# Performance work log

Measured on AMD Instinct MI355X. Metric: run time of the kernel, lower is better.

The kernel has to match this reference:

```python
import jax, jax.numpy as jnp
import numpy as np
from jax import lax

B, T = 64, 200
NUM_C, DIM_S, SIZE_M = 2000, 128, 50


def setup_inputs() -> dict:
    key = jax.random.key(0)
    ks = jax.random.split(key, 12)
    d = {}
    d['skill'] = jax.random.randint(ks[0], (B, T), 0, NUM_C)
    d['answer'] = jax.random.randint(ks[1], (B, T), 0, 2)
    s = 1.0 / np.sqrt(DIM_S)
    d['k_emb'] = jax.random.normal(ks[2], (NUM_C + 1, DIM_S), jnp.float32)
    d['v_emb'] = jax.random.normal(ks[3], (2 * NUM_C + 1, DIM_S), jnp.float32)
    # kaiming_normal on [size_m, dim_s]: std = sqrt(2/dim_s)
    d['Mk'] = jax.random.normal(ks[4], (SIZE_M, DIM_S), jnp.float32) * np.sqrt(2.0 / DIM_S)
    d['Mv0'] = jax.random.normal(ks[5], (SIZE_M, DIM_S), jnp.float32) * np.sqrt(2.0 / DIM_S)
    d['f_W'] = jax.random.normal(ks[6], (DIM_S, 2 * DIM_S), jnp.float32) * (1.0 / np.sqrt(2 * DIM_S))
    d['f_b'] = jnp.zeros((DIM_S,), jnp.float32)
    d['p_W'] = jax.random.normal(ks[7], (NUM_C, DIM_S), jnp.float32) * s
    d['p_b'] = jnp.zeros((NUM_C,), jnp.float32)
    d['e_W'] = jax.random.normal(ks[8], (DIM_S, DIM_S), jnp.float32) * s
    d['e_b'] = jnp.zeros((DIM_S,), jnp.float32)
    d['a_W'] = jax.random.normal(ks[9], (DIM_S, DIM_S), jnp.float32) * s
    d['a_b'] = jnp.zeros((DIM_S,), jnp.float32)
    return d


def reference(skill, answer, k_emb, v_emb, Mk, Mv0, f_W, f_b, p_W, p_b, e_W, e_b, a_W, a_b):
    num_c = p_W.shape[0]
    bsz = skill.shape[0]
    answer_x = jnp.where(answer == 2, 1, answer)
    x = skill + num_c * answer_x                       # [B,T]
    k = k_emb[skill]                                   # [B,T,D]
    v = v_emb[x]                                       # [B,T,D]
    w = jax.nn.softmax(jnp.einsum('btd,md->btm', k, Mk), axis=-1)   # [B,T,M]
    e = jax.nn.sigmoid(jnp.einsum('btd,ed->bte', v, e_W) + e_b)      # [B,T,D]
    a = jnp.tanh(jnp.einsum('btd,ed->bte', v, a_W) + a_b)            # [B,T,D]

    Mv_init = jnp.broadcast_to(Mv0, (bsz,) + Mv0.shape)              # [B,M,D]

    def step(Mvt, inp):
        et, at, wt = inp                               # [B,D],[B,D],[B,M]
        # read uses pre-update memory (Mv[:, :-1] in the torch code)
        read = jnp.einsum('bm,bmd->bd', wt, Mvt)
        Mvt_new = Mvt * (1.0 - wt[:, :, None] * et[:, None, :]) + wt[:, :, None] * at[:, None, :]
        return Mvt_new, read

    _, reads = lax.scan(step, Mv_init,
                        (e.transpose(1, 0, 2), a.transpose(1, 0, 2), w.transpose(1, 0, 2)))
    reads = reads.transpose(1, 0, 2)                   # [B,T,D]

    f = jnp.tanh(jnp.concatenate([reads, k], axis=-1) @ f_W.T + f_b)  # [B,T,D]
    p = jax.nn.sigmoid(f @ p_W.T + p_b)                # [B,T,num_c] (dropout is identity at eval)
    p = p[:, :-1, :]
    next_skill = skill[:, 1:]                          # [B,T-1]
    idx = jnp.minimum(next_skill, num_c - 1)
    pred = jnp.take_along_axis(p, idx[..., None], axis=-1)[..., 0]
    pred = jnp.where(next_skill < num_c, pred, 0.0)    # index num_c -> zero row in torch one_hot
    return pred
```

## Files before the change

### kernel.cpp

```cpp
#include <hip/hip_runtime.h>
#include <math.h>

#define Bsz 64
#define Tn 200
#define NUMC 2000
#define DS 128
#define SM 50
#define NTOK (Bsz*Tn)

typedef __attribute__((ext_vector_type(8))) short bfrag;
typedef __attribute__((ext_vector_type(4))) float f32x4;
typedef __attribute__((ext_vector_type(4))) unsigned int u32x4;

__device__ __forceinline__ unsigned short f2bf(float x) {
    unsigned int u = __builtin_bit_cast(unsigned int, x);
    u = u + 0x7fffu + ((u >> 16) & 1u);
    return (unsigned short)(u >> 16);
}
__device__ __forceinline__ unsigned int pack2(float a, float b) {
    return (unsigned int)f2bf(a) | ((unsigned int)f2bf(b) << 16);
}
__device__ __forceinline__ bfrag mk_frag(f32x4 x, f32x4 y) {
    u32x4 t;
    t[0] = pack2(x[0], x[1]); t[1] = pack2(x[2], x[3]);
    t[2] = pack2(y[0], y[1]); t[3] = pack2(y[2], y[3]);
    return __builtin_bit_cast(bfrag, t);
}

__device__ __forceinline__ float fast_exp(float x)  { return __builtin_amdgcn_exp2f(x * 1.44269504f); }
__device__ __forceinline__ float fast_rcp(float x)  { return __builtin_amdgcn_rcpf(x); }
__device__ __forceinline__ float fast_sigmoid(float x) { return fast_rcp(1.f + fast_exp(-x)); }
__device__ __forceinline__ float fast_tanh(float x) { return 1.f - 2.f * fast_rcp(fast_exp(2.f * x) + 1.f); }

__global__ __launch_bounds__(256) void k0_cast(
    const float* __restrict__ eW, const float* __restrict__ aW,
    const float* __restrict__ fW, const float* __restrict__ Mk,
    unsigned int* __restrict__ BeaU, unsigned int* __restrict__ BkmU,
    unsigned int* __restrict__ Bf0U)
{
    const int g = blockIdx.x * 256 + threadIdx.x;
    if (g >= 9216) return;
    int gm, mat;
    unsigned int* dst;
    if (g < 4096)      { mat = 0; gm = g;        dst = BeaU; }
    else if (g < 7168) { mat = 1; gm = g - 4096; dst = BkmU; }
    else               { mat = 2; gm = g - 7168; dst = Bf0U; }
    const int nt = gm >> 8, r = gm & 255, ki = r >> 6, L = r & 63;
    const int n = nt * 16 + (L & 15);
    const int k = ki * 32 + (L >> 4) * 8;

    const float* src = nullptr;
    if (mat == 0) {
        src = (n < 128) ? (eW + (size_t)n * DS + k) : (aW + (size_t)(n - 128) * DS + k);
    } else if (mat == 1) {
        if (n < 128)      src = fW + (size_t)n * (2 * DS) + DS + k;
        else if (n < 128 + SM) src = Mk + (size_t)(n - 128) * DS + k;
    } else {
        src = fW + (size_t)n * (2 * DS) + k;
    }
    float v[8];
    #pragma unroll
    for (int j = 0; j < 8; j++) v[j] = src ? src[j] : 0.f;
    u32x4 o;
    o[0] = pack2(v[0], v[1]); o[1] = pack2(v[2], v[3]);
    o[2] = pack2(v[4], v[5]); o[3] = pack2(v[6], v[7]);
    ((u32x4*)dst)[gm] = o;
}

__global__ __launch_bounds__(64, 4) void k1_gemm(
    const int* __restrict__ skill, const int* __restrict__ answer,
    const float* __restrict__ k_emb, const float* __restrict__ v_emb,
    const unsigned int* __restrict__ BeaU, const unsigned int* __restrict__ BkmU,
    const float* __restrict__ eB, const float* __restrict__ aB,
    float* __restrict__ w2, float* __restrict__ e_buf,
    float* __restrict__ a_buf, float* __restrict__ kp_buf)
{
    const int bid = blockIdx.x;
    const int tile = bid / 7, role = bid % 7;
    const int L = threadIdx.x, L15 = L & 15, quad = L >> 4;
    const int tok0 = tile * 16;
    const int tokA = tok0 + L15;
    const int row0 = tok0 + quad * 4;

    const int s = skill[tokA];
    const float* ap;
    if (role < 4) {
        const int an = answer[tokA];
        const int ax = (an == 2) ? 1 : an;
        ap = v_emb + ((size_t)(s + NUMC * ax)) * DS + quad * 8;
    } else {
        ap = k_emb + (size_t)s * DS + quad * 8;
    }
    bfrag Af[4];
    #pragma unroll
    for (int ki = 0; ki < 4; ki++) {
        const f32x4* a4 = (const f32x4*)(ap + ki * 32);
        Af[ki] = mk_frag(a4[0], a4[1]);
    }

    const bfrag* Bp = (role < 4) ? (const bfrag*)BeaU : (const bfrag*)BkmU;
    const int g0 = (role < 4) ? role * 4 : (role - 4) * 4;

    f32x4 acc[4];
    #pragma unroll
    for (int t = 0; t < 4; t++) acc[t] = (f32x4){0.f,0.f,0.f,0.f};

    #pragma unroll
    for (int half = 0; half < 2; half++) {
        bfrag bh[2][4];
        #pragma unroll
        for (int tt = 0; tt < 2; tt++)
            #pragma unroll
            for (int ki = 0; ki < 4; ki++)
                bh[tt][ki] = Bp[(size_t)((g0 + half * 2 + tt) * 4 + ki) * 64 + L];
        #pragma unroll
        for (int ki = 0; ki < 4; ki++)
            #pragma unroll
            for (int tt = 0; tt < 2; tt++)
                acc[half * 2 + tt] = __builtin_amdgcn_mfma_f32_16x16x32_bf16(
                    Af[ki], bh[tt][ki], acc[half * 2 + tt], 0, 0, 0);
    }

    if (role == 6) {
        #pragma unroll
        for (int reg = 0; reg < 4; reg++) {
            float mx = -1e30f;
            #pragma unroll
            for (int t = 0; t < 4; t++) { const int c = t * 16 + L15; if (c < SM) mx = fmaxf(mx, acc[t][reg]); }
            #pragma unroll
            for (int msk = 1; msk <= 8; msk <<= 1) mx = fmaxf(mx, __shfl_xor(mx, msk));
            float ex[4]; float ssum = 0.f;
            #pragma unroll
            for (int t = 0; t < 4; t++) {
                const int c = t * 16 + L15;
                ex[t] = (c < SM) ? fast_exp(acc[t][reg] - mx) : 0.f;
                ssum += ex[t];
            }
            #pragma unroll
            for (int msk = 1; msk <= 8; msk <<= 1) ssum += __shfl_xor(ssum, msk);
            const float inv = fast_rcp(ssum);
            float* wp = w2 + (size_t)(row0 + reg) * 64;
            #pragma unroll
            for (int t = 0; t < 4; t++) {
                const int c = t * 16 + L15;
                wp[c] = ex[t] * inv;
            }
        }
    } else {
        const int nb = (role & 1) * 64;
        float* obuf = (role < 2) ? e_buf : (role < 4) ? a_buf : kp_buf;
        const float* bias = (role < 2) ? eB : aB;
        #pragma unroll
        for (int t = 0; t < 4; t++) {
            const int n = nb + t * 16 + L15;
            const float bv = (role < 4) ? bias[n] : 0.f;
            #pragma unroll
            for (int reg = 0; reg < 4; reg++) {
                float v = acc[t][reg] + bv;
                if (role < 2)      v = fast_sigmoid(v);
                else if (role < 4) v = fast_tanh(v);
                obuf[(size_t)(row0 + reg) * DS + n] = v;
            }
        }
    }
}

__global__ __launch_bounds__(64) void k2_scan(
    const float* __restrict__ w2, const float* __restrict__ e_buf,
    const float* __restrict__ a_buf, const float* __restrict__ Mv0,
    unsigned short* __restrict__ reads)
{
    const int bid  = blockIdx.x;
    const int b    = bid >> 5;
    const int dseg = bid & 31;
    const int lane = threadIdx.x;
    const int mg   = lane >> 2;
    const int dd   = lane & 3;
    const int d    = dseg * 4 + dd;
    const int m0   = mg * 4;
    const int base = b * Tn;

    float Mv[4];
    #pragma unroll
    for (int j = 0; j < 4; j++) {
        const int m = (m0 + j < SM) ? (m0 + j) : (SM - 1);
        Mv[j] = Mv0[(size_t)m * DS + d];
    }

    float ev[4][4], av[4][4];
    f32x4 wv[4][4];

    #define LOADS(S, T0)                                                       \
        { _Pragma("unroll")                                                    \
          for (int i_ = 0; i_ < 4; i_++) {                                     \
              const int t_ = (T0) + i_;                                        \
              const int tc_ = (t_ < Tn) ? t_ : 0;                              \
              ev[S][i_] = e_buf[(size_t)(base + tc_) * DS + d];                \
              av[S][i_] = a_buf[(size_t)(base + tc_) * DS + d];                \
              wv[S][i_] = *(const f32x4*)(w2 + (size_t)(base + tc_) * 64 + m0);\
          } }

    #define PROC4(S, T0)                                                       \
        { float r4[4];                                                         \
          _Pragma("unroll")                                                    \
          for (int it = 0; it < 4; it++) {                                     \
              const float ev_ = ev[S][it], av_ = av[S][it];                    \
              float rd = 0.f;                                                  \
              _Pragma("unroll")                                                \
              for (int j = 0; j < 4; j++) {                                    \
                  const float wm = wv[S][it][j];                               \
                  rd = fmaf(wm, Mv[j], rd);                        \
                  Mv[j] = fmaf(-wm, fmaf(ev_, Mv[j], -av_), Mv[j]);            \
              }                                                                \
              rd += __shfl_xor(rd, 4);                                         \
              rd += __shfl_xor(rd, 8);                                         \
              rd += __shfl_xor(rd, 16);                                        \
              rd += __shfl_xor(rd, 32);                                        \
              r4[it] = rd;                                                     \
          }                                                                    \
          if (mg < 4) {                                                        \
              const float val = (mg == 0) ? r4[0] : (mg == 1) ? r4[1]          \
                              : (mg == 2) ? r4[2] : r4[3];                     \
              reads[(size_t)(base + (T0) + mg) * DS + d] = f2bf(val);          \
          } }

    LOADS(0, 0) LOADS(1, 4) LOADS(2, 8) LOADS(3, 12)

    for (int blk = 0; blk < 12; blk++) {
        const int t0 = blk * 16;
        PROC4(0, t0)      LOADS(0, t0 + 16)
        PROC4(1, t0 + 4)  LOADS(1, t0 + 20)
        PROC4(2, t0 + 8)  LOADS(2, t0 + 24)
        PROC4(3, t0 + 12) LOADS(3, t0 + 28)
    }
    PROC4(0, 192)
    PROC4(1, 196)
    #undef LOADS
    #undef PROC4
}

__global__ __launch_bounds__(128, 2) void k3_gemm(
    const unsigned short* __restrict__ reads, const float* __restrict__ kp_buf,
    const unsigned int* __restrict__ Bf0U, const float* __restrict__ fB,
    const float* __restrict__ pW, const float* __restrict__ pB,
    const int* __restrict__ skill, float* __restrict__ out)
{
    const int tid = threadIdx.x;
    const int wv  = tid >> 6;
    const int L   = tid & 63, L15 = L & 15, quad = L >> 4;
    const int tok0 = blockIdx.x * 16;
    const int tokA = tok0 + L15;
    const int row0 = tok0 + quad * 4;

    __shared__ float sm[2][16];

    bfrag Rf[4];
    #pragma unroll
    for (int ki = 0; ki < 4; ki++)
        Rf[ki] = *(const bfrag*)(reads + (size_t)tokA * DS + ki * 32 + quad * 8);

    const bfrag* Bf0 = (const bfrag*)Bf0U;
    const int g0 = wv * 4;

    f32x4 acc[4];
    #pragma unroll
    for (int t = 0; t < 4; t++) acc[t] = (f32x4){0.f,0.f,0.f,0.f};

    #pragma unroll
    for (int half = 0; half < 2; half++) {
        bfrag bh[2][4];
        #pragma unroll
        for (int tt = 0; tt < 2; tt++)
            #pragma unroll
            for (int ki = 0; ki < 4; ki++)
                bh[tt][ki] = Bf0[(size_t)((g0 + half * 2 + tt) * 4 + ki) * 64 + L];
        #pragma unroll
        for (int ki = 0; ki < 4; ki++)
            #pragma unroll
            for (int tt = 0; tt < 2; tt++)
                acc[half * 2 + tt] = __builtin_amdgcn_mfma_f32_16x16x32_bf16(
                    Rf[ki], bh[tt][ki], acc[half * 2 + tt], 0, 0, 0);
    }

    const int nb = wv * 64;
    float f[4][4];
    #pragma unroll
    for (int t = 0; t < 4; t++) {
        const int n = nb + t * 16 + L15;
        const float fb = fB[n];
        #pragma unroll
        for (int reg = 0; reg < 4; reg++)
            f[reg][t] = fast_tanh(acc[t][reg] + kp_buf[(size_t)(row0 + reg) * DS + n] + fb);
    }

    #pragma unroll
    for (int reg = 0; reg < 4; reg++) {
        const int tok = row0 + reg;
        const int t = tok % Tn;
        const bool act = (t < Tn - 1);
        float contrib = 0.f;
        if (act) {
            const int sn = skill[tok + 1];
            const int ix = (sn < NUMC) ? sn : (NUMC - 1);
            const float* pr = pW + (size_t)ix * DS + nb + L15;
            #pragma unroll
            for (int t4 = 0; t4 < 4; t4++)
                contrib = fmaf(f[reg][t4], pr[t4 * 16], contrib);
        }
        #pragma unroll
        for (int msk = 1; msk <= 8; msk <<= 1)
            contrib += __shfl_xor(contrib, msk);
        if (L15 == 0) sm[wv][quad * 4 + reg] = contrib;
    }
    __syncthreads();
    if (tid < 16) {
        const int tok = tok0 + tid;
        const int t = tok % Tn;
        if (t < Tn - 1) {
            const int sn = skill[tok + 1];
            const int ix = (sn < NUMC) ? sn : (NUMC - 1);
            const float val = sm[0][tid] + sm[1][tid] + pB[ix];
            out[(size_t)(tok / Tn) * (Tn - 1) + t] = (sn < NUMC) ? fast_sigmoid(val) : 0.f;
        }
    }
}

extern "C" void kernel_launch(void* const* d_in, const int* in_sizes, int n_in,
                              void* d_out, int out_size, void* d_ws, size_t ws_size,
                              hipStream_t stream)
{
    const int*   skill  = (const int*)  d_in[0];
    const int*   answer = (const int*)  d_in[1];
    const float* k_emb  = (const float*)d_in[2];
    const float* v_emb  = (const float*)d_in[3];
    const float* Mk     = (const float*)d_in[4];
    const float* Mv0    = (const float*)d_in[5];
    const float* f_W    = (const float*)d_in[6];
    const float* f_b    = (const float*)d_in[7];
    const float* p_W    = (const float*)d_in[8];
    const float* p_b    = (const float*)d_in[9];
    const float* e_W    = (const float*)d_in[10];
    const float* e_b    = (const float*)d_in[11];
    const float* a_W    = (const float*)d_in[12];
    const float* a_b    = (const float*)d_in[13];
    float* out = (float*)d_out;

    float* ws     = (float*)d_ws;
    float* w2     = ws;
    float* e_buf  = w2     + (size_t)NTOK*64;
    float* a_buf  = e_buf  + (size_t)NTOK*DS;
    float* kp_buf = a_buf  + (size_t)NTOK*DS;
    unsigned short* reads = (unsigned short*)(kp_buf + (size_t)NTOK*DS);
    unsigned int* BeaU = (unsigned int*)(reads + (size_t)NTOK*DS);
    unsigned int* BkmU = BeaU + 4096 * 4;
    unsigned int* Bf0U = BkmU + 3072 * 4;

    k0_cast<<<36, 256, 0, stream>>>(e_W, a_W, f_W, Mk, BeaU, BkmU, Bf0U);
    k1_gemm<<<7*(NTOK/16), 64, 0, stream>>>(skill, answer, k_emb, v_emb,
        BeaU, BkmU, e_b, a_b, w2, e_buf, a_buf, kp_buf);
    k2_scan<<<Bsz*32, 64, 0, stream>>>(w2, e_buf, a_buf, Mv0, reads);
    k3_gemm<<<NTOK/16, 128, 0, stream>>>(reads, kp_buf, Bf0U, f_b,
        p_W, p_b, skill, out);
}
```

Before: 134.2 us.

## Split memory scan into time chunks with affine prefix composition

The sequential memory-update scan over 200 timesteps is split into 4 time chunks. A first kernel computes each chunk's per-element affine transform (P, Q), and a second kernel composes the earlier chunks' transforms to get that chunk's starting memory, then runs the chunk's scan and emits reads. This shortens the serial dependency chain per block and raises block count. In exchange it adds an extra pass over e/a/w inputs, P/Q buffers in workspace, and an extra kernel launch.

After: 155.1 us. 15.6% more time.

```diff
diff --git a/kernel.cpp b/kernel.cpp
--- a/kernel.cpp
+++ b/kernel.cpp
@@ -7,6 +7,8 @@
 #define DS 128
 #define SM 50
 #define NTOK (Bsz*Tn)
+#define NCH 4
+#define CHL 52
 
 typedef __attribute__((ext_vector_type(8))) short bfrag;
 typedef __attribute__((ext_vector_type(4))) float f32x4;
@@ -165,30 +167,31 @@
     }
 }
 
-__global__ __launch_bounds__(64) void k2_scan(
+
+__global__ __launch_bounds__(64) void k2a_prod(
     const float* __restrict__ w2, const float* __restrict__ e_buf,
-    const float* __restrict__ a_buf, const float* __restrict__ Mv0,
-    unsigned short* __restrict__ reads)
+    const float* __restrict__ a_buf,
+    float* __restrict__ Pbuf, float* __restrict__ Qbuf)
 {
     const int bid  = blockIdx.x;
-    const int b    = bid >> 5;
-    const int dseg = bid & 31;
+    const int b    = bid >> 6;
+    const int r    = bid & 63;
+    const int dseg = r >> 2;
+    const int c    = r & 3;
     const int lane = threadIdx.x;
-    const int mg   = lane >> 2;
-    const int dd   = lane & 3;
-    const int d    = dseg * 4 + dd;
-    const int m0   = mg * 4;
+    const int mg   = lane >> 3;
+    const int dd   = lane & 7;
+    const int d    = dseg * 8 + dd;
     const int base = b * Tn;
-
-    float Mv[4];
-    #pragma unroll
-    for (int j = 0; j < 4; j++) {
-        const int m = (m0 + j < SM) ? (m0 + j) : (SM - 1);
-        Mv[j] = Mv0[(size_t)m * DS + d];
-    }
-
-    float ev[4][4], av[4][4];
-    f32x4 wv[4][4];
+    const int s    = c * CHL;
+    const int npair = (c < 3) ? 6 : 5;
+
+    float P[8], Q[8];
+    #pragma unroll
+    for (int j = 0; j < 8; j++) { P[j] = 1.f; Q[j] = 0.f; }
+
+    float ev[2][4], av[2][4];
+    f32x4 wva[2][4], wvb[2][4];
 
     #define LOADS(S, T0)                                                       \
         { _Pragma("unroll")                                                    \
@@ -197,7 +200,89 @@
               const int tc_ = (t_ < Tn) ? t_ : 0;                              \
               ev[S][i_] = e_buf[(size_t)(base + tc_) * DS + d];                \
               av[S][i_] = a_buf[(size_t)(base + tc_) * DS + d];                \
-              wv[S][i_] = *(const f32x4*)(w2 + (size_t)(base + tc_) * 64 + m0);\
+              const float* wp_ = w2 + (size_t)(base + tc_) * 64 + mg * 8;      \
+              wva[S][i_] = *(const f32x4*)wp_;                                 \
+              wvb[S][i_] = *(const f32x4*)(wp_ + 4);                           \
+          } }
+
+    #define PROC4A(S)                                                          \
+        { _Pragma("unroll")                                                    \
+          for (int it = 0; it < 4; it++) {                                     \
+              const float ev_ = ev[S][it], av_ = av[S][it];                    \
+              _Pragma("unroll")                                                \
+              for (int j = 0; j < 8; j++) {                                    \
+                  const float wm = (j < 4) ? wva[S][it][j] : wvb[S][it][j-4];  \
+                  const float tmp = wm * ev_;                                  \
+                  P[j] = fmaf(-tmp, P[j], P[j]);                               \
+                  Q[j] = fmaf(-tmp, Q[j], Q[j]);                               \
+                  Q[j] = fmaf(wm, av_, Q[j]);                                  \
+              } } }
+
+    LOADS(0, s) LOADS(1, s + 4)
+    int t0 = s;
+    for (int i = 0; i < npair; i++) {
+        PROC4A(0) LOADS(0, t0 + 8)
+        PROC4A(1) LOADS(1, t0 + 12)
+        t0 += 8;
+    }
+    PROC4A(0)
+
+    #pragma unroll
+    for (int j = 0; j < 8; j++) {
+        const size_t idx = (((size_t)c * Bsz + b) * 64 + mg * 8 + j) * DS + d;
+        Pbuf[idx] = P[j];
+        Qbuf[idx] = Q[j];
+    }
+    #undef LOADS
+    #undef PROC4A
+}
+
+__global__ __launch_bounds__(64) void k2b_scan(
+    const float* __restrict__ w2, const float* __restrict__ e_buf,
+    const float* __restrict__ a_buf, const float* __restrict__ Mv0,
+    const float* __restrict__ Pbuf, const float* __restrict__ Qbuf,
+    unsigned short* __restrict__ reads)
+{
+    const int bid  = blockIdx.x;
+    const int b    = bid >> 6;
+    const int r    = bid & 63;
+    const int dseg = r >> 2;
+    const int c    = r & 3;
+    const int lane = threadIdx.x;
+    const int mg   = lane >> 3;
+    const int dd   = lane & 7;
+    const int d    = dseg * 8 + dd;
+    const int base = b * Tn;
+    const int s    = c * CHL;
+    const int npair = (c < 3) ? 6 : 5;
+
+    float Mv[8];
+    #pragma unroll
+    for (int j = 0; j < 8; j++) {
+        const int m = mg * 8 + j;
+        Mv[j] = Mv0[(size_t)((m < SM) ? m : (SM - 1)) * DS + d];
+    }
+    for (int cc = 0; cc < c; cc++) {
+        #pragma unroll
+        for (int j = 0; j < 8; j++) {
+            const size_t idx = (((size_t)cc * Bsz + b) * 64 + mg * 8 + j) * DS + d;
+            Mv[j] = fmaf(Pbuf[idx], Mv[j], Qbuf[idx]);
+        }
+    }
+
+    float ev[2][4], av[2][4];
+    f32x4 wva[2][4], wvb[2][4];
+
+    #define LOADS(S, T0)                                                       \
+        { _Pragma("unroll")                                                    \
+          for (int i_ = 0; i_ < 4; i_++) {                                     \
+              const int t_ = (T0) + i_;                                        \
+              const int tc_ = (t_ < Tn) ? t_ : 0;                              \
+              ev[S][i_] = e_buf[(size_t)(base + tc_) * DS + d];                \
+              av[S][i_] = a_buf[(size_t)(base + tc_) * DS + d];                \
+              const float* wp_ = w2 + (size_t)(base + tc_) * 64 + mg * 8;      \
+              wva[S][i_] = *(const f32x4*)wp_;                                 \
+              wvb[S][i_] = *(const f32x4*)(wp_ + 4);                           \
           } }
 
     #define PROC4(S, T0)                                                       \
@@ -207,12 +292,11 @@
               const float ev_ = ev[S][it], av_ = av[S][it];                    \
               float rd = 0.f;                                                  \
               _Pragma("unroll")                                                \
-              for (int j = 0; j < 4; j++) {                                    \
-                  const float wm = wv[S][it][j];                               \
+              for (int j = 0; j < 8; j++) {                                    \
+                  const float wm = (j < 4) ? wva[S][it][j] : wvb[S][it][j-4];  \
                   rd = fmaf(wm, Mv[j], rd);                        \
                   Mv[j] = fmaf(-wm, fmaf(ev_, Mv[j], -av_), Mv[j]);            \
               }                                                                \
-              rd += __shfl_xor(rd, 4);                                         \
               rd += __shfl_xor(rd, 8);                                         \
               rd += __shfl_xor(rd, 16);                                        \
               rd += __shfl_xor(rd, 32);                                        \
@@ -224,17 +308,14 @@
               reads[(size_t)(base + (T0) + mg) * DS + d] = f2bf(val);          \
           } }
 
-    LOADS(0, 0) LOADS(1, 4) LOADS(2, 8) LOADS(3, 12)
-
-    for (int blk = 0; blk < 12; blk++) {
-        const int t0 = blk * 16;
-        PROC4(0, t0)      LOADS(0, t0 + 16)
-        PROC4(1, t0 + 4)  LOADS(1, t0 + 20)
-        PROC4(2, t0 + 8)  LOADS(2, t0 + 24)
-        PROC4(3, t0 + 12) LOADS(3, t0 + 28)
-    }
-    PROC4(0, 192)
-    PROC4(1, 196)
+    LOADS(0, s) LOADS(1, s + 4)
+    int t0 = s;
+    for (int i = 0; i < npair; i++) {
+        PROC4(0, t0)     LOADS(0, t0 + 8)
+        PROC4(1, t0 + 4) LOADS(1, t0 + 12)
+        t0 += 8;
+    }
+    PROC4(0, t0)
     #undef LOADS
     #undef PROC4
 }
@@ -351,14 +432,17 @@
     float* a_buf  = e_buf  + (size_t)NTOK*DS;
     float* kp_buf = a_buf  + (size_t)NTOK*DS;
     unsigned short* reads = (unsigned short*)(kp_buf + (size_t)NTOK*DS);
-    unsigned int* BeaU = (unsigned int*)(reads + (size_t)NTOK*DS);
+    float* Pbuf   = (float*)(reads + (size_t)NTOK*DS);
+    float* Qbuf   = Pbuf   + (size_t)NCH*Bsz*64*DS;
+    unsigned int* BeaU = (unsigned int*)(Qbuf + (size_t)NCH*Bsz*64*DS);
     unsigned int* BkmU = BeaU + 4096 * 4;
     unsigned int* Bf0U = BkmU + 3072 * 4;
 
     k0_cast<<<36, 256, 0, stream>>>(e_W, a_W, f_W, Mk, BeaU, BkmU, Bf0U);
     k1_gemm<<<7*(NTOK/16), 64, 0, stream>>>(skill, answer, k_emb, v_emb,
         BeaU, BkmU, e_b, a_b, w2, e_buf, a_buf, kp_buf);
-    k2_scan<<<Bsz*32, 64, 0, stream>>>(w2, e_buf, a_buf, Mv0, reads);
+    k2a_prod<<<Bsz*64, 64, 0, stream>>>(w2, e_buf, a_buf, Pbuf, Qbuf);
+    k2b_scan<<<Bsz*64, 64, 0, stream>>>(w2, e_buf, a_buf, Mv0, Pbuf, Qbuf, reads);
     k3_gemm<<<NTOK/16, 128, 0, stream>>>(reads, kp_buf, Bf0U, f_b,
         p_W, p_b, skill, out);
 }
```
